# Optimization experiments

Measured on AMD Instinct MI355X. Metric: run time of the kernel, lower is better.

Reference implementation:

```python
import jax, jax.numpy as jnp
import numpy as np

D_MODEL = 512
D_STATE = 16
D_CONV = 4
EXPAND = 2
D_INNER = EXPAND * D_MODEL  # 1024
DT_RANK = D_MODEL // 16     # 32 (ceil(512/16))
BATCH, SEQ = 8, 1024


def setup_inputs() -> dict:
    key = jax.random.key(0)
    ks = jax.random.split(key, 10)
    w = lambda i, shape, s=0.02: (jax.random.normal(ks[i], shape, jnp.float32) * s)
    return {
        "x": jax.random.normal(ks[0], (BATCH, SEQ, D_MODEL), jnp.float32),
        # Mamba params
        "W_in": w(1, (2 * D_INNER, D_MODEL)),            # in_proj (no bias)
        "conv_w": w(2, (D_INNER, D_CONV), 0.1),          # depthwise causal conv
        "conv_b": jnp.zeros((D_INNER,), jnp.float32),
        "W_x": w(3, (DT_RANK + 2 * D_STATE, D_INNER)),   # x_proj (no bias)
        "W_dt": w(4, (D_INNER, DT_RANK)),                # dt_proj
        "b_dt": jnp.full((D_INNER,), -4.6, jnp.float32), # -> softplus ~ 0.01
        "A_log": jnp.log(jnp.broadcast_to(
            jnp.arange(1, D_STATE + 1, dtype=jnp.float32), (D_INNER, D_STATE))),
        "D": jnp.ones((D_INNER,), jnp.float32),
        "W_out": w(5, (D_MODEL, D_INNER)),               # out_proj (no bias)
        # LayerNorm + head
        "ln_g": jnp.ones((D_MODEL,), jnp.float32),
        "ln_b": jnp.zeros((D_MODEL,), jnp.float32),
        "head_W": w(6, (D_MODEL, D_MODEL)),
        "head_b": jnp.zeros((D_MODEL,), jnp.float32),
    }


def reference(x, W_in, conv_w, conv_b, W_x, W_dt, b_dt, A_log, D, W_out,
              ln_g, ln_b, head_W, head_b):
    B, L, _ = x.shape
    # in_proj -> split into x branch and gate z
    xz = x @ W_in.T                               # (B, L, 2*D_INNER)
    xi, z = jnp.split(xz, 2, axis=-1)
    # causal depthwise conv1d over time (pad left d_conv-1), then SiLU
    xp = jnp.pad(xi, ((0, 0), (D_CONV - 1, 0), (0, 0)))
    xc = conv_b + sum(conv_w[:, k] * xp[:, k:k + L, :] for k in range(D_CONV))
    xc = jax.nn.silu(xc)                          # (B, L, D_INNER)
    # x_proj -> dt, B, C
    dbc = xc @ W_x.T
    dt = jax.nn.softplus(dbc[..., :DT_RANK] @ W_dt.T + b_dt)   # (B, L, D_INNER)
    Bm = dbc[..., DT_RANK:DT_RANK + D_STATE]                   # (B, L, D_STATE)
    Cm = dbc[..., DT_RANK + D_STATE:]                          # (B, L, D_STATE)
    A = -jnp.exp(A_log)                                        # (D_INNER, D_STATE)

    def step(h, ins):
        dt_t, B_t, C_t, u_t = ins                 # (B,Din) (B,Ds) (B,Ds) (B,Din)
        dA = jnp.exp(dt_t[:, :, None] * A)        # (B, Din, Ds)
        h = dA * h + (dt_t * u_t)[:, :, None] * B_t[:, None, :]
        y = jnp.einsum('bds,bs->bd', h, C_t)
        return h, y

    h0 = jnp.zeros((B, D_INNER, D_STATE), x.dtype)
    xs = (dt.transpose(1, 0, 2), Bm.transpose(1, 0, 2),
          Cm.transpose(1, 0, 2), xc.transpose(1, 0, 2))
    _, ys = jax.lax.scan(step, h0, xs)            # ys: (L, B, D_INNER)
    y = ys.transpose(1, 0, 2) + D * xc
    y = y * jax.nn.silu(z)
    out = y @ W_out.T                             # (B, L, D_MODEL)
    # LayerNorm is per-token, so norm the last token only (== LN(out)[:, -1])
    last = out[:, -1, :]
    mu = last.mean(-1, keepdims=True)
    var = ((last - mu) ** 2).mean(-1, keepdims=True)
    lastn = (last - mu) / jnp.sqrt(var + 1e-5) * ln_g + ln_b
    return lastn @ head_W.T + head_b              # (B, D_MODEL)
```

## Files before the change

kernel.cpp:

```cpp
#include <hip/hip_runtime.h>
#include <stdint.h>

#define B_   8
#define L_   1024
#define DM   512
#define DI   1024
#define DS   16
#define DTR  32
#define M_   (B_*L_)

typedef short v8s __attribute__((ext_vector_type(8)));
typedef short v4s __attribute__((ext_vector_type(4)));
typedef float v4f __attribute__((ext_vector_type(4)));

static __device__ __forceinline__ short f2bf(float f) {
  union { float f; uint32_t u; } v; v.f = f;
  uint32_t r = v.u + 0x7FFFu + ((v.u >> 16) & 1u);
  return (short)(r >> 16);
}
static __device__ __forceinline__ float bf2f(short s) {
  union { uint32_t u; float f; } v; v.u = ((uint32_t)(uint16_t)s) << 16; return v.f;
}
static __device__ __forceinline__ float silu_fast(float a) {
  return a * __builtin_amdgcn_rcpf(1.f + __expf(-a));
}
static __device__ __forceinline__ float wsum(float v) {
#pragma unroll
  for (int o = 32; o > 0; o >>= 1) v += __shfl_xor(v, o, 64);
  return v;
}
static __device__ __forceinline__ void gl_lds16(const short* g, short* l) {
  __builtin_amdgcn_global_load_lds(
      (const __attribute__((address_space(1))) void*)g,
      (__attribute__((address_space(3))) void*)l, 16, 0, 0);
}

__global__ __launch_bounds__(256) void k_prep(const float* __restrict__ x,
                                              const float* __restrict__ w_in,
                                              const float* __restrict__ w_x,
                                              const float* __restrict__ w_dt,
                                              const float* __restrict__ a_log,
                                              short* xb, short* wib, short* wxb, short* wdtb,
                                              float* Aneg, float* zlast) {
  if (blockIdx.x >= 4704) {
    int w = (int)(blockIdx.x - 4704) * 4 + (threadIdx.x >> 6);
    int l = threadIdx.x & 63;
    int b = w >> 10, j = w & 1023;
    const v4f* xr = (const v4f*)(x + ((size_t)(b * L_ + L_ - 1)) * DM);
    const v4f* wr = (const v4f*)(w_in + (size_t)(DI + j) * DM);
    float s = 0.f;
#pragma unroll
    for (int i = 0; i < 2; ++i) {
      v4f a = xr[l + 64 * i], c = wr[l + 64 * i];
      s += a[0]*c[0] + a[1]*c[1] + a[2]*c[2] + a[3]*c[3];
    }
    s = wsum(s);
    if (l == 0) zlast[b * DI + j] = s;
    return;
  }
  int idx = (blockIdx.x * 256 + threadIdx.x) * 4;
  const int n0 = M_ * DM, n1 = DI * DM, n2 = 48 * DI, n3 = DI * DTR, n4 = DI * DS;
  const float* src; short* dst;
  if (idx < n0)              { src = x + idx;    dst = xb + idx; }
  else if ((idx -= n0) < n1) { src = w_in + idx; dst = wib + idx; }
  else if ((idx -= n1) < n2) { src = w_x + idx;  dst = wxb + idx; }
  else if ((idx -= n2) < n3) { src = w_dt + idx; dst = wdtb + idx; }
  else if ((idx -= n3) < n4) {
    v4f v = *(const v4f*)(a_log + idx);
    v4f o;
#pragma unroll
    for (int i = 0; i < 4; ++i) o[i] = -__expf(v[i]);
    *(v4f*)(Aneg + idx) = o;
    return;
  }
  else return;
  v4f v = *(const v4f*)src;
  v4s o;
#pragma unroll
  for (int i = 0; i < 4; ++i) o[i] = f2bf(v[i]);
  *(v4s*)dst = o;
}

__global__ __launch_bounds__(256) void k_gemm_xi(const short* __restrict__ xb,
                                                 const short* __restrict__ wib,
                                                 short* __restrict__ xib) {
  __shared__ short sh[128 * 136];
  short* lA = sh;
  short* lB = sh + 128 * 64;
  int mb = blockIdx.x >> 3, nb = blockIdx.x & 7;
  int tid = threadIdx.x;
  int w = tid >> 6, l = tid & 63, lm = l & 15, q = l >> 4;
  int wm = (w >> 1) * 64, wn = (w & 1) * 64;

  v4f acc[4][4];
#pragma unroll
  for (int i = 0; i < 4; ++i)
#pragma unroll
    for (int j = 0; j < 4; ++j) acc[i][j] = (v4f){0,0,0,0};

  int srow_in_chunk = l >> 3;
  int sslot = l & 7;
  const short* Abase = xb  + (size_t)(mb * 128) * DM;
  const short* Bbase = wib + (size_t)(nb * 128) * DM;

  for (int k0 = 0; k0 < DM; k0 += 64) {
    if (k0) __syncthreads();
#pragma unroll
    for (int i = 0; i < 4; ++i) {
      int chunk = w * 4 + i;
      int row = chunk * 8 + srow_in_chunk;
      int c = sslot ^ (row & 7);
      gl_lds16(Abase + (size_t)row * DM + k0 + c * 8, lA + chunk * 512);
      gl_lds16(Bbase + (size_t)row * DM + k0 + c * 8, lB + chunk * 512);
    }
    __syncthreads();
#pragma unroll
    for (int kt = 0; kt < 2; ++kt) {
      v8s af[4], bf[4];
      int p = (kt * 4 + q) ^ (lm & 7);
#pragma unroll
      for (int t = 0; t < 4; ++t) {
        af[t] = *(const v8s*)(lA + (wm + t * 16 + lm) * 64 + p * 8);
        bf[t] = *(const v8s*)(lB + (wn + t * 16 + lm) * 64 + p * 8);
      }
#pragma unroll
      for (int i = 0; i < 4; ++i)
#pragma unroll
        for (int j = 0; j < 4; ++j)
          acc[i][j] = __builtin_amdgcn_mfma_f32_16x16x32_bf16(af[i], bf[j], acc[i][j], 0, 0, 0);
    }
  }
  __syncthreads();
#pragma unroll
  for (int i = 0; i < 4; ++i)
#pragma unroll
    for (int r = 0; r < 4; ++r) {
      int row = wm + i * 16 + q * 4 + r;
#pragma unroll
      for (int j = 0; j < 4; ++j)
        sh[row * 136 + wn + j * 16 + lm] = f2bf(acc[i][j][r]);
    }
  __syncthreads();
  int cc = tid & 15;
#pragma unroll
  for (int g = 0; g < 8; ++g) {
    int rr = (tid >> 4) + g * 16;
    v8s v = *(const v8s*)(sh + rr * 136 + cc * 8);
    *(v8s*)(xib + (size_t)(mb * 128 + rr) * DI + nb * 128 + cc * 8) = v;
  }
}

__global__ __launch_bounds__(256) void k_conv(const short* __restrict__ xib,
                                              const float* __restrict__ conv_w,
                                              const float* __restrict__ conv_b,
                                              short* __restrict__ xcb,
                                              float* __restrict__ xclast) {
  int bid = blockIdx.x;
  int b = bid >> 7, tc = bid & 127;
  int tid = threadIdx.x;
  int d8 = tid & 127, th = tid >> 7;
  int d = d8 * 8;
  int t0 = tc * 8 + th * 4;
  v4f cw[8];
  float cb[8];
#pragma unroll
  for (int i = 0; i < 8; ++i) {
    cw[i] = *(const v4f*)(conv_w + (d + i) * 4);
    cb[i] = conv_b[d + i];
  }
  float w0[8], w1[8], w2[8];
  const short* base = xib + (size_t)(b * L_) * DI + d;
  short* obase = xcb + (size_t)(b * L_) * DI + d;
#pragma unroll
  for (int i = 0; i < 8; ++i) { w0[i] = 0.f; w1[i] = 0.f; w2[i] = 0.f; }
  if (t0 >= 3) {
    v8s v0 = *(const v8s*)(base + (size_t)(t0 - 3) * DI);
    v8s v1 = *(const v8s*)(base + (size_t)(t0 - 2) * DI);
    v8s v2 = *(const v8s*)(base + (size_t)(t0 - 1) * DI);
#pragma unroll
    for (int i = 0; i < 8; ++i) { w0[i] = bf2f(v0[i]); w1[i] = bf2f(v1[i]); w2[i] = bf2f(v2[i]); }
  }
#pragma unroll
  for (int t = t0; t < t0 + 4; ++t) {
    v8s cur = *(const v8s*)(base + (size_t)t * DI);
    v8s ob;
#pragma unroll
    for (int i = 0; i < 8; ++i) {
      float xv = bf2f(cur[i]);
      float a = cb[i] + cw[i][0] * w0[i] + cw[i][1] * w1[i] + cw[i][2] * w2[i] + cw[i][3] * xv;
      float s = silu_fast(a);
      ob[i] = f2bf(s);
      if (t == L_ - 1) xclast[b * DI + d + i] = s;
      w0[i] = w1[i]; w1[i] = w2[i]; w2[i] = xv;
    }
    *(v8s*)(obase + (size_t)t * DI) = ob;
  }
}

__global__ __launch_bounds__(256) void k_dbcdt(const short* __restrict__ xcb,
                                               const short* __restrict__ wxb,
                                               const short* __restrict__ wdtb,
                                               const float* __restrict__ b_dt,
                                               float* __restrict__ Bmat,
                                               _Float16* __restrict__ dtO,
                                               float* __restrict__ csum2) {
  __shared__ float red[4 * 16 * 49];
  __shared__ short ta[16 * 32];
  int m = blockIdx.x;
  int tid = threadIdx.x, w = tid >> 6, l = tid & 63, lm = l & 15, q = l >> 4;
  v4f a0 = {0,0,0,0}, a1 = {0,0,0,0}, a2 = {0,0,0,0};
  const short* ap = xcb + (size_t)(m * 16 + lm) * DI + w * 256 + q * 8;
  const short* b0 = wxb + (size_t)lm * DI        + w * 256 + q * 8;
  const short* b1 = wxb + (size_t)(16 + lm) * DI + w * 256 + q * 8;
  const short* b2 = wxb + (size_t)(32 + lm) * DI + w * 256 + q * 8;
#pragma unroll
  for (int kk = 0; kk < 8; ++kk) {
    v8s a = *(const v8s*)(ap + kk * 32);
    a0 = __builtin_amdgcn_mfma_f32_16x16x32_bf16(a, *(const v8s*)(b0 + kk * 32), a0, 0, 0, 0);
    a1 = __builtin_amdgcn_mfma_f32_16x16x32_bf16(a, *(const v8s*)(b1 + kk * 32), a1, 0, 0, 0);
    a2 = __builtin_amdgcn_mfma_f32_16x16x32_bf16(a, *(const v8s*)(b2 + kk * 32), a2, 0, 0, 0);
  }
#pragma unroll
  for (int r = 0; r < 4; ++r) {
    int row = q * 4 + r;
    red[w * 784 + row * 49 + lm]      = a0[r];
    red[w * 784 + row * 49 + 16 + lm] = a1[r];
    red[w * 784 + row * 49 + 32 + lm] = a2[r];
  }
  __syncthreads();
  {
    int row = tid >> 4, c0 = tid & 15;
    int base = row * 49 + c0;
    float s0 = red[base] + red[784 + base] + red[1568 + base] + red[2352 + base];
    float s1 = red[base + 16] + red[784 + base + 16] + red[1568 + base + 16] + red[2352 + base + 16];
    float s2 = red[base + 32] + red[784 + base + 32] + red[1568 + base + 32] + red[2352 + base + 32];
    ta[row * 32 + c0]      = f2bf(s0);
    ta[row * 32 + 16 + c0] = f2bf(s1);
    Bmat[(size_t)(m * 16 + row) * DS + c0] = s2;
  }
  __syncthreads();
  v8s ad = *(const v8s*)(ta + lm * 32 + q * 8);
#pragma unroll 4
  for (int nn = 0; nn < 16; ++nn) {
    int nt = w * 16 + nn;
    v8s bb = *(const v8s*)(wdtb + (size_t)(nt * 16 + lm) * DTR + q * 8);
    v4f zz = {0,0,0,0};
    v4f dd = __builtin_amdgcn_mfma_f32_16x16x32_bf16(ad, bb, zz, 0, 0, 0);
    int col = nt * 16 + lm;
    float bd = b_dt[col];
    float s = 0.f;
#pragma unroll
    for (int r = 0; r < 4; ++r) {
      float v = dd[r] + bd;
      float sp = (v > 15.f) ? v : __logf(1.f + __expf(v));
      dtO[(size_t)(m * 16 + q * 4 + r) * DI + col] = (_Float16)sp;
      s += sp;
    }
    s += __shfl_xor(s, 16, 64);
    s += __shfl_xor(s, 32, 64);
    if (q == 0) csum2[(size_t)m * DI + col] = s;
  }
}

__global__ __launch_bounds__(256) void k_sufc(const float* __restrict__ csum2,
                                              const float* __restrict__ xclast,
                                              const float* __restrict__ w_x,
                                              float* __restrict__ SS,
                                              float* __restrict__ clast) {
  if (blockIdx.x < 32) {
    int b = blockIdx.x >> 2, dseg = blockIdx.x & 3;
    int d = dseg * 256 + threadIdx.x;
    float run = 0.f;
    for (int ch = 31; ch >= 0; --ch) {
      SS[(size_t)(b * 32 + ch) * DI + d] = run;
      run += csum2[(size_t)(b * 64 + 2 * ch + 1) * DI + d]
           + csum2[(size_t)(b * 64 + 2 * ch) * DI + d];
    }
  } else {
    int w2 = (int)(blockIdx.x - 32) * 4 + (threadIdx.x >> 6);
    int l = threadIdx.x & 63;
    int b = w2 >> 4, ss = w2 & 15;
    const v4f* xr = (const v4f*)(xclast + (size_t)b * DI);
    const v4f* wr = (const v4f*)(w_x + (size_t)(48 + ss) * DI);
    float s = 0.f;
#pragma unroll
    for (int i = 0; i < 4; ++i) {
      v4f a = xr[l + 64 * i], c = wr[l + 64 * i];
      s += a[0]*c[0] + a[1]*c[1] + a[2]*c[2] + a[3]*c[3];
    }
    s = wsum(s);
    if (l == 0) clast[b * 16 + ss] = s;
  }
}

__global__ __launch_bounds__(256) void k_scan(const _Float16* __restrict__ dt,
                                              const short* __restrict__ xcb,
                                              const float* __restrict__ Bmat,
                                              const float* __restrict__ SS,
                                              const float* __restrict__ Aneg,
                                              const float* __restrict__ clast,
                                              float* __restrict__ ypart) {
  __shared__ float lB[32 * 16];
  int bid = blockIdx.x;
  int b = bid >> 7, ch = (bid >> 2) & 31, dg = bid & 3;
  int tid = threadIdx.x;
  for (int i = tid; i < 32 * 16; i += 256)
    lB[i] = Bmat[(size_t)(b * L_ + ch * 32) * DS + i];
  __syncthreads();
  int d = dg * 256 + tid;
  float S = SS[(size_t)(b * 32 + ch) * DI + d];
  float As2[16];
#pragma unroll
  for (int s = 0; s < 16; ++s) As2[s] = Aneg[d * 16 + s] * 1.44269504f;
  float h[16];
#pragma unroll
  for (int s = 0; s < 16; ++s) h[s] = 0.f;
  const _Float16* dtp = dt + ((size_t)(b * L_ + ch * 32)) * DI + d;
  const short* xcp = xcb + ((size_t)(b * L_ + ch * 32)) * DI + d;
  for (int tl = 31; tl >= 0; --tl) {
    float dtv = (float)dtp[(size_t)tl * DI];
    float u   = bf2f(xcp[(size_t)tl * DI]);
    float c = dtv * u;
#pragma unroll
    for (int s = 0; s < 16; ++s)
      h[s] += __builtin_amdgcn_exp2f(As2[s] * S) * (c * lB[tl * 16 + s]);
    S += dtv;
  }
  float yp = 0.f;
#pragma unroll
  for (int s = 0; s < 16; ++s) yp += h[s] * clast[b * 16 + s];
  ypart[(size_t)(b * 32 + ch) * DI + d] = yp;
}

__global__ __launch_bounds__(256) void k_ylast(const float* __restrict__ ypart,
                                               const float* __restrict__ xclast,
                                               const float* __restrict__ Dp,
                                               const float* __restrict__ zlast,
                                               float* __restrict__ ylast) {
  int idx = blockIdx.x * 256 + threadIdx.x;
  int b = idx >> 10, d = idx & 1023;
  float acc = 0.f;
#pragma unroll 8
  for (int ch = 0; ch < 32; ++ch) acc += ypart[(size_t)(b * 32 + ch) * DI + d];
  float y = acc + Dp[d] * xclast[idx];
  ylast[idx] = y * silu_fast(zlast[idx]);
}

__global__ __launch_bounds__(256) void k_out(const float* __restrict__ ylast,
                                             const float* __restrict__ w_out,
                                             float* __restrict__ olast) {
  int w = blockIdx.x * 4 + (threadIdx.x >> 6);
  int l = threadIdx.x & 63;
  int b = w >> 9, i = w & 511;
  const v4f* yr = (const v4f*)(ylast + (size_t)b * DI);
  const v4f* wr = (const v4f*)(w_out + (size_t)i * DI);
  float s = 0.f;
#pragma unroll
  for (int k = 0; k < 4; ++k) {
    v4f a = yr[l + 64 * k], c = wr[l + 64 * k];
    s += a[0]*c[0] + a[1]*c[1] + a[2]*c[2] + a[3]*c[3];
  }
  s = wsum(s);
  if (l == 0) olast[b * DM + i] = s;
}

__global__ __launch_bounds__(256) void k_ln(const float* __restrict__ olast,
                                            const float* __restrict__ g,
                                            const float* __restrict__ be,
                                            float* __restrict__ lastn) {
  __shared__ float s1[256], s2[256];
  int b = blockIdx.x, tid = threadIdx.x;
  float v0 = olast[b * DM + tid], v1 = olast[b * DM + 256 + tid];
  s1[tid] = v0 + v1; s2[tid] = v0 * v0 + v1 * v1;
  __syncthreads();
  for (int o = 128; o > 0; o >>= 1) {
    if (tid < o) { s1[tid] += s1[tid + o]; s2[tid] += s2[tid + o]; }
    __syncthreads();
  }
  float mu = s1[0] / (float)DM;
  float var = s2[0] / (float)DM - mu * mu;
  float inv = 1.f / sqrtf(var + 1e-5f);
  lastn[b * DM + tid]       = (v0 - mu) * inv * g[tid]       + be[tid];
  lastn[b * DM + 256 + tid] = (v1 - mu) * inv * g[tid + 256] + be[tid + 256];
}

__global__ __launch_bounds__(256) void k_head(const float* __restrict__ lastn,
                                              const float* __restrict__ hw,
                                              const float* __restrict__ hb,
                                              float* __restrict__ out) {
  int w = blockIdx.x * 4 + (threadIdx.x >> 6);
  int l = threadIdx.x & 63;
  int b = w >> 9, o = w & 511;
  const v4f* xr = (const v4f*)(lastn + (size_t)b * DM);
  const v4f* wr = (const v4f*)(hw + (size_t)o * DM);
  float s = 0.f;
#pragma unroll
  for (int k = 0; k < 2; ++k) {
    v4f a = xr[l + 64 * k], c = wr[l + 64 * k];
    s += a[0]*c[0] + a[1]*c[1] + a[2]*c[2] + a[3]*c[3];
  }
  s = wsum(s);
  if (l == 0) out[b * DM + o] = s + hb[o];
}

extern "C" void kernel_launch(void* const* d_in, const int* in_sizes, int n_in,
                              void* d_out, int out_size, void* d_ws, size_t ws_size,
                              hipStream_t stream) {
  const float* x      = (const float*)d_in[0];
  const float* w_in   = (const float*)d_in[1];
  const float* conv_w = (const float*)d_in[2];
  const float* conv_b = (const float*)d_in[3];
  const float* w_x    = (const float*)d_in[4];
  const float* w_dt   = (const float*)d_in[5];
  const float* b_dt   = (const float*)d_in[6];
  const float* a_log  = (const float*)d_in[7];
  const float* Dp     = (const float*)d_in[8];
  const float* w_out  = (const float*)d_in[9];
  const float* ln_g   = (const float*)d_in[10];
  const float* ln_b   = (const float*)d_in[11];
  const float* head_W = (const float*)d_in[12];
  const float* head_b = (const float*)d_in[13];
  float* out = (float*)d_out;

  char* ws = (char*)d_ws;
  size_t off = 0;
  auto alloc = [&](size_t bytes) { void* p = ws + off; off += (bytes + 255) & ~(size_t)255; return p; };
  short* xb     = (short*)alloc((size_t)M_*DM*2);
  short* wib    = (short*)alloc((size_t)DI*DM*2);
  short* wxb    = (short*)alloc((size_t)48*DI*2);
  short* wdtb   = (short*)alloc((size_t)DI*DTR*2);
  float* Aneg   = (float*)alloc((size_t)DI*DS*4);
  short* xib    = (short*)alloc((size_t)M_*DI*2);
  short* xcb    = (short*)alloc((size_t)M_*DI*2);
  _Float16* dt  = (_Float16*)alloc((size_t)M_*DI*2);
  float* Bmat   = (float*)alloc((size_t)M_*DS*4);
  float* csum2  = (float*)alloc((size_t)512*DI*4);
  float* SS     = (float*)alloc((size_t)B_*32*DI*4);
  float* ypart  = (float*)alloc((size_t)B_*32*DI*4);
  float* zlast  = (float*)alloc((size_t)B_*DI*4);
  float* clast  = (float*)alloc((size_t)B_*DS*4);
  float* xclast = (float*)alloc((size_t)B_*DI*4);
  float* ylast  = (float*)alloc((size_t)B_*DI*4);
  float* olast  = (float*)alloc((size_t)B_*DM*4);
  float* lastn  = (float*)alloc((size_t)B_*DM*4);

  k_prep<<<6752, 256, 0, stream>>>(x, w_in, w_x, w_dt, a_log, xb, wib, wxb, wdtb, Aneg, zlast);
  k_gemm_xi<<<512, 256, 0, stream>>>(xb, wib, xib);
  k_conv<<<1024, 256, 0, stream>>>(xib, conv_w, conv_b, xcb, xclast);
  k_dbcdt<<<512, 256, 0, stream>>>(xcb, wxb, wdtb, b_dt, Bmat, dt, csum2);
  k_sufc<<<64, 256, 0, stream>>>(csum2, xclast, w_x, SS, clast);
  k_scan<<<1024, 256, 0, stream>>>(dt, xcb, Bmat, SS, Aneg, clast, ypart);
  k_ylast<<<32, 256, 0, stream>>>(ypart, xclast, Dp, zlast, ylast);
  k_out<<<1024, 256, 0, stream>>>(ylast, w_out, olast);
  k_ln<<<8, 256, 0, stream>>>(olast, ln_g, ln_b, lastn);
  k_head<<<1024, 256, 0, stream>>>(lastn, head_W, head_b, out);
}
```

Baseline: 178.8 us.

## Use 8 waves in xi GEMM and fold suffix sums into scan

The in-projection GEMM now runs 512 threads per block. Each of 8 waves computes a 64x32 subtile instead of a 64x64 one, and LDS loads and stores are spread over more threads. The separate suffix-sum pass over csum2 is removed. Each scan block now sums the later chunk totals itself, and the C-last dot product becomes its own small kernel. This trades a serial suffix kernel and an SS buffer round trip for redundant reads of csum2 in the scan blocks, up to 62 rows per thread.

After: 186.9 us. +4.5%, slower.

```diff
diff --git a/kernel.cpp b/kernel.cpp
--- a/kernel.cpp
+++ b/kernel.cpp
@@ -81,7 +81,7 @@
   *(v4s*)dst = o;
 }
 
-__global__ __launch_bounds__(256) void k_gemm_xi(const short* __restrict__ xb,
+__global__ __launch_bounds__(512) void k_gemm_xi(const short* __restrict__ xb,
                                                  const short* __restrict__ wib,
                                                  short* __restrict__ xib) {
   __shared__ short sh[128 * 136];
@@ -90,13 +90,13 @@
   int mb = blockIdx.x >> 3, nb = blockIdx.x & 7;
   int tid = threadIdx.x;
   int w = tid >> 6, l = tid & 63, lm = l & 15, q = l >> 4;
-  int wm = (w >> 1) * 64, wn = (w & 1) * 64;
-
-  v4f acc[4][4];
+  int wm = (w >> 2) * 64, wn = (w & 3) * 32;
+
+  v4f acc[4][2];
 #pragma unroll
   for (int i = 0; i < 4; ++i)
 #pragma unroll
-    for (int j = 0; j < 4; ++j) acc[i][j] = (v4f){0,0,0,0};
+    for (int j = 0; j < 2; ++j) acc[i][j] = (v4f){0,0,0,0};
 
   int srow_in_chunk = l >> 3;
   int sslot = l & 7;
@@ -106,8 +106,8 @@
   for (int k0 = 0; k0 < DM; k0 += 64) {
     if (k0) __syncthreads();
 #pragma unroll
-    for (int i = 0; i < 4; ++i) {
-      int chunk = w * 4 + i;
+    for (int i = 0; i < 2; ++i) {
+      int chunk = w * 2 + i;
       int row = chunk * 8 + srow_in_chunk;
       int c = sslot ^ (row & 7);
       gl_lds16(Abase + (size_t)row * DM + k0 + c * 8, lA + chunk * 512);
@@ -116,17 +116,18 @@
     __syncthreads();
 #pragma unroll
     for (int kt = 0; kt < 2; ++kt) {
-      v8s af[4], bf[4];
+      v8s af[4], bf[2];
       int p = (kt * 4 + q) ^ (lm & 7);
 #pragma unroll
-      for (int t = 0; t < 4; ++t) {
+      for (int t = 0; t < 4; ++t)
         af[t] = *(const v8s*)(lA + (wm + t * 16 + lm) * 64 + p * 8);
+#pragma unroll
+      for (int t = 0; t < 2; ++t)
         bf[t] = *(const v8s*)(lB + (wn + t * 16 + lm) * 64 + p * 8);
-      }
 #pragma unroll
       for (int i = 0; i < 4; ++i)
 #pragma unroll
-        for (int j = 0; j < 4; ++j)
+        for (int j = 0; j < 2; ++j)
           acc[i][j] = __builtin_amdgcn_mfma_f32_16x16x32_bf16(af[i], bf[j], acc[i][j], 0, 0, 0);
     }
   }
@@ -137,14 +138,14 @@
     for (int r = 0; r < 4; ++r) {
       int row = wm + i * 16 + q * 4 + r;
 #pragma unroll
-      for (int j = 0; j < 4; ++j)
+      for (int j = 0; j < 2; ++j)
         sh[row * 136 + wn + j * 16 + lm] = f2bf(acc[i][j][r]);
     }
   __syncthreads();
   int cc = tid & 15;
 #pragma unroll
-  for (int g = 0; g < 8; ++g) {
-    int rr = (tid >> 4) + g * 16;
+  for (int g = 0; g < 4; ++g) {
+    int rr = (tid >> 4) + g * 32;
     v8s v = *(const v8s*)(sh + rr * 136 + cc * 8);
     *(v8s*)(xib + (size_t)(mb * 128 + rr) * DI + nb * 128 + cc * 8) = v;
   }
@@ -262,41 +263,28 @@
   }
 }
 
-__global__ __launch_bounds__(256) void k_sufc(const float* __restrict__ csum2,
-                                              const float* __restrict__ xclast,
-                                              const float* __restrict__ w_x,
-                                              float* __restrict__ SS,
-                                              float* __restrict__ clast) {
-  if (blockIdx.x < 32) {
-    int b = blockIdx.x >> 2, dseg = blockIdx.x & 3;
-    int d = dseg * 256 + threadIdx.x;
-    float run = 0.f;
-    for (int ch = 31; ch >= 0; --ch) {
-      SS[(size_t)(b * 32 + ch) * DI + d] = run;
-      run += csum2[(size_t)(b * 64 + 2 * ch + 1) * DI + d]
-           + csum2[(size_t)(b * 64 + 2 * ch) * DI + d];
-    }
-  } else {
-    int w2 = (int)(blockIdx.x - 32) * 4 + (threadIdx.x >> 6);
-    int l = threadIdx.x & 63;
-    int b = w2 >> 4, ss = w2 & 15;
-    const v4f* xr = (const v4f*)(xclast + (size_t)b * DI);
-    const v4f* wr = (const v4f*)(w_x + (size_t)(48 + ss) * DI);
-    float s = 0.f;
-#pragma unroll
-    for (int i = 0; i < 4; ++i) {
-      v4f a = xr[l + 64 * i], c = wr[l + 64 * i];
-      s += a[0]*c[0] + a[1]*c[1] + a[2]*c[2] + a[3]*c[3];
-    }
-    s = wsum(s);
-    if (l == 0) clast[b * 16 + ss] = s;
-  }
+__global__ __launch_bounds__(256) void k_clast(const float* __restrict__ xclast,
+                                               const float* __restrict__ w_x,
+                                               float* __restrict__ clast) {
+  int w2 = (int)blockIdx.x * 4 + (threadIdx.x >> 6);
+  int l = threadIdx.x & 63;
+  int b = w2 >> 4, ss = w2 & 15;
+  const v4f* xr = (const v4f*)(xclast + (size_t)b * DI);
+  const v4f* wr = (const v4f*)(w_x + (size_t)(48 + ss) * DI);
+  float s = 0.f;
+#pragma unroll
+  for (int i = 0; i < 4; ++i) {
+    v4f a = xr[l + 64 * i], c = wr[l + 64 * i];
+    s += a[0]*c[0] + a[1]*c[1] + a[2]*c[2] + a[3]*c[3];
+  }
+  s = wsum(s);
+  if (l == 0) clast[b * 16 + ss] = s;
 }
 
 __global__ __launch_bounds__(256) void k_scan(const _Float16* __restrict__ dt,
                                               const short* __restrict__ xcb,
                                               const float* __restrict__ Bmat,
-                                              const float* __restrict__ SS,
+                                              const float* __restrict__ csum2,
                                               const float* __restrict__ Aneg,
                                               const float* __restrict__ clast,
                                               float* __restrict__ ypart) {
@@ -308,7 +296,9 @@
     lB[i] = Bmat[(size_t)(b * L_ + ch * 32) * DS + i];
   __syncthreads();
   int d = dg * 256 + tid;
-  float S = SS[(size_t)(b * 32 + ch) * DI + d];
+  float S = 0.f;
+  for (int m = 2 * ch + 2; m < 64; ++m)
+    S += csum2[(size_t)(b * 64 + m) * DI + d];
   float As2[16];
 #pragma unroll
   for (int s = 0; s < 16; ++s) As2[s] = Aneg[d * 16 + s] * 1.44269504f;
@@ -435,7 +425,6 @@
   _Float16* dt  = (_Float16*)alloc((size_t)M_*DI*2);
   float* Bmat   = (float*)alloc((size_t)M_*DS*4);
   float* csum2  = (float*)alloc((size_t)512*DI*4);
-  float* SS     = (float*)alloc((size_t)B_*32*DI*4);
   float* ypart  = (float*)alloc((size_t)B_*32*DI*4);
   float* zlast  = (float*)alloc((size_t)B_*DI*4);
   float* clast  = (float*)alloc((size_t)B_*DS*4);
@@ -445,11 +434,11 @@
   float* lastn  = (float*)alloc((size_t)B_*DM*4);
 
   k_prep<<<6752, 256, 0, stream>>>(x, w_in, w_x, w_dt, a_log, xb, wib, wxb, wdtb, Aneg, zlast);
-  k_gemm_xi<<<512, 256, 0, stream>>>(xb, wib, xib);
+  k_gemm_xi<<<512, 512, 0, stream>>>(xb, wib, xib);
   k_conv<<<1024, 256, 0, stream>>>(xib, conv_w, conv_b, xcb, xclast);
   k_dbcdt<<<512, 256, 0, stream>>>(xcb, wxb, wdtb, b_dt, Bmat, dt, csum2);
-  k_sufc<<<64, 256, 0, stream>>>(csum2, xclast, w_x, SS, clast);
-  k_scan<<<1024, 256, 0, stream>>>(dt, xcb, Bmat, SS, Aneg, clast, ypart);
+  k_clast<<<32, 256, 0, stream>>>(xclast, w_x, clast);
+  k_scan<<<1024, 256, 0, stream>>>(dt, xcb, Bmat, csum2, Aneg, clast, ypart);
   k_ylast<<<32, 256, 0, stream>>>(ypart, xclast, Dp, zlast, ylast);
   k_out<<<1024, 256, 0, stream>>>(ylast, w_out, olast);
   k_ln<<<8, 256, 0, stream>>>(olast, ln_g, ln_b, lastn);
```

## Fold suffix-sum and clast into neighbours, fuse LayerNorm with head

Applied to the files above, without the earlier changes.

Removes the k_sufc kernel. The clast dot products now run as 32 extra blocks of k_dbcdt, and each k_scan block recomputes its chunk's suffix sum of dt directly from csum2 instead of reading a precomputed SS buffer. LayerNorm is merged into the head GEMV, with every block recomputing the per-batch norm in shared memory. This saves two kernel launches and their inter-kernel gaps, at the cost of redundant work: up to 62 extra csum2 loads per scan thread and 128 redundant LayerNorm computations per batch.

New measurement: 185.5 us. 3.8% more time.

```diff
diff --git a/kernel.cpp b/kernel.cpp
--- a/kernel.cpp
+++ b/kernel.cpp
@@ -201,9 +201,28 @@
                                                const short* __restrict__ wxb,
                                                const short* __restrict__ wdtb,
                                                const float* __restrict__ b_dt,
+                                               const float* __restrict__ xclast,
+                                               const float* __restrict__ w_x,
                                                float* __restrict__ Bmat,
                                                _Float16* __restrict__ dtO,
-                                               float* __restrict__ csum2) {
+                                               float* __restrict__ csum2,
+                                               float* __restrict__ clast) {
+  if (blockIdx.x >= 512) {
+    int w2 = (int)(blockIdx.x - 512) * 4 + (threadIdx.x >> 6);
+    int l = threadIdx.x & 63;
+    int b = w2 >> 4, ss = w2 & 15;
+    const v4f* xr = (const v4f*)(xclast + (size_t)b * DI);
+    const v4f* wr = (const v4f*)(w_x + (size_t)(48 + ss) * DI);
+    float s = 0.f;
+#pragma unroll
+    for (int i = 0; i < 4; ++i) {
+      v4f a = xr[l + 64 * i], c = wr[l + 64 * i];
+      s += a[0]*c[0] + a[1]*c[1] + a[2]*c[2] + a[3]*c[3];
+    }
+    s = wsum(s);
+    if (l == 0) clast[b * 16 + ss] = s;
+    return;
+  }
   __shared__ float red[4 * 16 * 49];
   __shared__ short ta[16 * 32];
   int m = blockIdx.x;
@@ -262,41 +281,10 @@
   }
 }
 
-__global__ __launch_bounds__(256) void k_sufc(const float* __restrict__ csum2,
-                                              const float* __restrict__ xclast,
-                                              const float* __restrict__ w_x,
-                                              float* __restrict__ SS,
-                                              float* __restrict__ clast) {
-  if (blockIdx.x < 32) {
-    int b = blockIdx.x >> 2, dseg = blockIdx.x & 3;
-    int d = dseg * 256 + threadIdx.x;
-    float run = 0.f;
-    for (int ch = 31; ch >= 0; --ch) {
-      SS[(size_t)(b * 32 + ch) * DI + d] = run;
-      run += csum2[(size_t)(b * 64 + 2 * ch + 1) * DI + d]
-           + csum2[(size_t)(b * 64 + 2 * ch) * DI + d];
-    }
-  } else {
-    int w2 = (int)(blockIdx.x - 32) * 4 + (threadIdx.x >> 6);
-    int l = threadIdx.x & 63;
-    int b = w2 >> 4, ss = w2 & 15;
-    const v4f* xr = (const v4f*)(xclast + (size_t)b * DI);
-    const v4f* wr = (const v4f*)(w_x + (size_t)(48 + ss) * DI);
-    float s = 0.f;
-#pragma unroll
-    for (int i = 0; i < 4; ++i) {
-      v4f a = xr[l + 64 * i], c = wr[l + 64 * i];
-      s += a[0]*c[0] + a[1]*c[1] + a[2]*c[2] + a[3]*c[3];
-    }
-    s = wsum(s);
-    if (l == 0) clast[b * 16 + ss] = s;
-  }
-}
-
 __global__ __launch_bounds__(256) void k_scan(const _Float16* __restrict__ dt,
                                               const short* __restrict__ xcb,
                                               const float* __restrict__ Bmat,
-                                              const float* __restrict__ SS,
+                                              const float* __restrict__ csum2,
                                               const float* __restrict__ Aneg,
                                               const float* __restrict__ clast,
                                               float* __restrict__ ypart) {
@@ -308,7 +296,9 @@
     lB[i] = Bmat[(size_t)(b * L_ + ch * 32) * DS + i];
   __syncthreads();
   int d = dg * 256 + tid;
-  float S = SS[(size_t)(b * 32 + ch) * DI + d];
+  float S = 0.f;
+  for (int m = 2 * ch + 2; m < 64; ++m)
+    S += csum2[(size_t)(b * 64 + m) * DI + d];
   float As2[16];
 #pragma unroll
   for (int s = 0; s < 16; ++s) As2[s] = Aneg[d * 16 + s] * 1.44269504f;
@@ -364,34 +354,33 @@
   if (l == 0) olast[b * DM + i] = s;
 }
 
-__global__ __launch_bounds__(256) void k_ln(const float* __restrict__ olast,
-                                            const float* __restrict__ g,
-                                            const float* __restrict__ be,
-                                            float* __restrict__ lastn) {
-  __shared__ float s1[256], s2[256];
-  int b = blockIdx.x, tid = threadIdx.x;
+__global__ __launch_bounds__(256) void k_ln_head(const float* __restrict__ olast,
+                                                 const float* __restrict__ g,
+                                                 const float* __restrict__ be,
+                                                 const float* __restrict__ hw,
+                                                 const float* __restrict__ hb,
+                                                 float* __restrict__ out) {
+  __shared__ float sn[DM];
+  __shared__ float r1[256], r2[256];
+  int bid = blockIdx.x, tid = threadIdx.x;
+  int b = bid >> 7;
   float v0 = olast[b * DM + tid], v1 = olast[b * DM + 256 + tid];
-  s1[tid] = v0 + v1; s2[tid] = v0 * v0 + v1 * v1;
+  r1[tid] = v0 + v1; r2[tid] = v0 * v0 + v1 * v1;
   __syncthreads();
   for (int o = 128; o > 0; o >>= 1) {
-    if (tid < o) { s1[tid] += s1[tid + o]; s2[tid] += s2[tid + o]; }
+    if (tid < o) { r1[tid] += r1[tid + o]; r2[tid] += r2[tid + o]; }
     __syncthreads();
   }
-  float mu = s1[0] / (float)DM;
-  float var = s2[0] / (float)DM - mu * mu;
+  float mu = r1[0] / (float)DM;
+  float var = r2[0] / (float)DM - mu * mu;
   float inv = 1.f / sqrtf(var + 1e-5f);
-  lastn[b * DM + tid]       = (v0 - mu) * inv * g[tid]       + be[tid];
-  lastn[b * DM + 256 + tid] = (v1 - mu) * inv * g[tid + 256] + be[tid + 256];
-}
-
-__global__ __launch_bounds__(256) void k_head(const float* __restrict__ lastn,
-                                              const float* __restrict__ hw,
-                                              const float* __restrict__ hb,
-                                              float* __restrict__ out) {
-  int w = blockIdx.x * 4 + (threadIdx.x >> 6);
-  int l = threadIdx.x & 63;
-  int b = w >> 9, o = w & 511;
-  const v4f* xr = (const v4f*)(lastn + (size_t)b * DM);
+  sn[tid]       = (v0 - mu) * inv * g[tid]       + be[tid];
+  sn[tid + 256] = (v1 - mu) * inv * g[tid + 256] + be[tid + 256];
+  __syncthreads();
+  int w = bid * 4 + (tid >> 6);
+  int l = tid & 63;
+  int o = w & 511;
+  const v4f* xr = (const v4f*)sn;
   const v4f* wr = (const v4f*)(hw + (size_t)o * DM);
   float s = 0.f;
 #pragma unroll
@@ -435,23 +424,19 @@
   _Float16* dt  = (_Float16*)alloc((size_t)M_*DI*2);
   float* Bmat   = (float*)alloc((size_t)M_*DS*4);
   float* csum2  = (float*)alloc((size_t)512*DI*4);
-  float* SS     = (float*)alloc((size_t)B_*32*DI*4);
   float* ypart  = (float*)alloc((size_t)B_*32*DI*4);
   float* zlast  = (float*)alloc((size_t)B_*DI*4);
   float* clast  = (float*)alloc((size_t)B_*DS*4);
   float* xclast = (float*)alloc((size_t)B_*DI*4);
   float* ylast  = (float*)alloc((size_t)B_*DI*4);
   float* olast  = (float*)alloc((size_t)B_*DM*4);
-  float* lastn  = (float*)alloc((size_t)B_*DM*4);
 
   k_prep<<<6752, 256, 0, stream>>>(x, w_in, w_x, w_dt, a_log, xb, wib, wxb, wdtb, Aneg, zlast);
   k_gemm_xi<<<512, 256, 0, stream>>>(xb, wib, xib);
   k_conv<<<1024, 256, 0, stream>>>(xib, conv_w, conv_b, xcb, xclast);
-  k_dbcdt<<<512, 256, 0, stream>>>(xcb, wxb, wdtb, b_dt, Bmat, dt, csum2);
-  k_sufc<<<64, 256, 0, stream>>>(csum2, xclast, w_x, SS, clast);
-  k_scan<<<1024, 256, 0, stream>>>(dt, xcb, Bmat, SS, Aneg, clast, ypart);
+  k_dbcdt<<<544, 256, 0, stream>>>(xcb, wxb, wdtb, b_dt, xclast, w_x, Bmat, dt, csum2, clast);
+  k_scan<<<1024, 256, 0, stream>>>(dt, xcb, Bmat, csum2, Aneg, clast, ypart);
   k_ylast<<<32, 256, 0, stream>>>(ypart, xclast, Dp, zlast, ylast);
   k_out<<<1024, 256, 0, stream>>>(ylast, w_out, olast);
-  k_ln<<<8, 256, 0, stream>>>(olast, ln_g, ln_b, lastn);
-  k_head<<<1024, 256, 0, stream>>>(lastn, head_W, head_b, out);
-}
+  k_ln_head<<<1024, 256, 0, stream>>>(olast, ln_g, ln_b, head_W, head_b, out);
+}
```
